# Performance work log

Measured on AMD Instinct MI355X. Metric: run time of the kernel, lower is better.

Reference implementation:

```python
import jax, jax.numpy as jnp
import numpy as np

C = 128; HEADS = 8; GH = 32; GW = 32; B = 8; PD = 8  # PD = (dim//4)//4

def _conv(x, w, pad, dil=1, groups=1):
    return jax.lax.conv_general_dilated(
        x, w, (1, 1), [(pad[0], pad[0]), (pad[1], pad[1])],
        rhs_dilation=(dil, dil),
        dimension_numbers=('NCHW', 'OIHW', 'NCHW'),
        feature_group_count=groups)

def _lrelu(t):
    return jnp.where(t >= 0, t, 0.1 * t)

def _ln(t, g, b, eps=1e-5):
    m = jnp.mean(t, -1, keepdims=True)
    v = jnp.var(t, -1, keepdims=True)
    return (t - m) * jax.lax.rsqrt(v + eps) * g + b

def setup_inputs():
    rng = np.random.RandomState(0)
    f = lambda *s: jnp.asarray((rng.randn(*s) * 0.05).astype(np.float32))
    ones = lambda n: jnp.ones((n,), jnp.float32)
    zeros = lambda n: jnp.zeros((n,), jnp.float32)
    # Swin-style relative position index over the (GH, GW) group
    coords = np.stack(np.meshgrid(np.arange(GH), np.arange(GW), indexing='ij')).reshape(2, -1)
    rel = (coords[:, :, None] - coords[:, None, :]).transpose(1, 2, 0)
    rel[..., 0] += GH - 1; rel[..., 1] += GW - 1; rel[..., 0] *= 2 * GW - 1
    rel_idx = jnp.asarray(rel.sum(-1).astype(np.int32))  # [N, N]
    biases = np.stack(np.meshgrid(np.arange(1 - GH, GH), np.arange(1 - GW, GW), indexing='ij'))
    biases = jnp.asarray(biases.reshape(2, -1).T.astype(np.float32))  # [(2GH-1)*(2GW-1), 2]
    return dict(
        x=jnp.asarray(rng.rand(B, C, GH, GW).astype(np.float32)),
        conv1_w=f(C, C, 3, 3), conv2_w=f(C, C, 3, 3), conv3_w=f(C, C, 3, 3),
        convt_w=f(C, 3, 1, 1),
        rba_w=f(C, C, 3, 1), rba_b=zeros(C), rbb_w=f(C, C, 1, 3), rbb_b=zeros(C),
        pp_w=f(PD, 2), pp_b=zeros(PD),
        l1_g=ones(PD), l1_b=zeros(PD), l1_w=f(PD, PD), l1_b2=zeros(PD),
        l2_g=ones(PD), l2_b=zeros(PD), l2_w=f(PD, PD), l2_b2=zeros(PD),
        l3_g=ones(PD), l3_b=zeros(PD), l3_w=f(HEADS, PD), l3_b2=zeros(HEADS),
        qk_w=f(2 * C, C), qk_b=zeros(2 * C),
        v_w=f(C, C), v_b=zeros(C),
        proj_w=f(C, C), proj_b=zeros(C),
        fc1_w=f(C, C), fc1_b=zeros(C), fc2_w=f(C, C), fc2_b=zeros(C),
        biases=biases, rel_idx=rel_idx,
    )

def reference(x, conv1_w, conv2_w, conv3_w, convt_w, rba_w, rba_b, rbb_w, rbb_b,
              pp_w, pp_b, l1_g, l1_b, l1_w, l1_b2, l2_g, l2_b, l2_w, l2_b2,
              l3_g, l3_b, l3_w, l3_b2, qk_w, qk_b, v_w, v_b, proj_w, proj_b,
              fc1_w, fc1_b, fc2_w, fc2_b, biases, rel_idx):
    Bn, Cc, Hh, Ww = x.shape
    N = Hh * Ww
    hd = Cc // HEADS
    # FeaExtract: ResASPP (3 dilated 3x3 convs, grouped 1x1 merge) + residual
    b1 = _lrelu(_conv(x, conv1_w, (1, 1)))
    b2 = _lrelu(_conv(x, conv2_w, (3, 3), dil=3))
    b3 = _lrelu(_conv(x, conv3_w, (5, 5), dil=5))
    a = _conv(jnp.concatenate([b1, b2, b3], 1), convt_w, (0, 0), groups=Cc) + x
    # RB: (3,1) conv -> lrelu -> (1,3) conv + residual
    r = _lrelu(_conv(a, rba_w, (1, 0)) + rba_b[None, :, None, None])
    r = _conv(r, rbb_w, (0, 1)) + rbb_b[None, :, None, None]
    o0 = r + a
    # original uses in-place clamp_, so o0 is clamped before flattening
    o0 = jnp.clip(o0, 0.0, 1.0)
    E = o0.reshape(Bn, Cc, N).transpose(0, 2, 1)  # [B, N, C]
    qk = E @ qk_w.T + qk_b  # [B, N, 2C]
    q = qk[..., :Cc].reshape(Bn, N, HEADS, hd).transpose(0, 2, 1, 3)
    k = qk[..., Cc:].reshape(Bn, N, HEADS, hd).transpose(0, 2, 1, 3)
    v = (E @ v_w.T + v_b).reshape(Bn, N, HEADS, hd).transpose(0, 2, 1, 3)
    attn = jnp.einsum('bhid,bhjd->bhij', q * (hd ** -0.5), k)
    # DynamicPosBias MLP (residual=False): Linear(2,pd) -> [LN,ReLU,Linear] x2 -> LN,ReLU,Linear(pd,heads)
    p = biases @ pp_w.T + pp_b
    p = jax.nn.relu(_ln(p, l1_g, l1_b)) @ l1_w.T + l1_b2
    p = jax.nn.relu(_ln(p, l2_g, l2_b)) @ l2_w.T + l2_b2
    p = jax.nn.relu(_ln(p, l3_g, l3_b)) @ l3_w.T + l3_b2  # [L, heads]
    rpb = p[rel_idx]  # gather -> [N, N, heads]
    attn = attn + rpb.transpose(2, 0, 1)[None]
    attn = jax.nn.softmax(attn, axis=-1)
    y = jnp.einsum('bhij,bhjd->bhid', attn, v).transpose(0, 2, 1, 3).reshape(Bn, N, Cc) + E
    x_proj = y @ proj_w.T + proj_b
    h = jax.nn.gelu(x_proj @ fc1_w.T + fc1_b, approximate=False)
    return (h @ fc2_w.T + fc2_b) + y
```

## Files before the change

### kernel.cpp

```cpp
#include <hip/hip_runtime.h>
#include <hip/hip_bf16.h>

typedef __hip_bfloat16 bf16;
typedef __bf16 bf16x8 __attribute__((ext_vector_type(8)));
typedef float f32x4 __attribute__((ext_vector_type(4)));

#define Lb 3969

#define XP_F   0
#define WF_F   903168
#define WR_F   1124352
#define WG_F   1173504
#define BH_F   1222656
#define R1P_F  1222656
#define QKV_F  1222656
#define AP_F   2795520
#define YT_F   2795520
#define EB_F   3352576
#define XPT_F  3352576
#define H1T_F  0
#define RPB_F  3876864
#define FLAG_F 3908616
#define RT_F   3908624
#define VT_F   4416528

__device__ __forceinline__ float b2f(bf16 v) { return __bfloat162float(v); }
__device__ __forceinline__ bf16 f2b(float v) { return __float2bfloat16(v); }

template <typename T> __device__ __forceinline__ float ldw(const void* p, int i);
template <> __device__ __forceinline__ float ldw<bf16>(const void* p, int i) {
  return __bfloat162float(((const bf16*)p)[i]);
}
template <> __device__ __forceinline__ float ldw<float>(const void* p, int i) {
  return ((const float*)p)[i];
}
template <typename T> __device__ __forceinline__ void stw(void* p, size_t i, float v);
template <> __device__ __forceinline__ void stw<bf16>(void* p, size_t i, float v) {
  ((bf16*)p)[i] = __float2bfloat16(v);
}
template <> __device__ __forceinline__ void stw<float>(void* p, size_t i, float v) {
  ((float*)p)[i] = v;
}

__device__ __forceinline__ unsigned pkb(float a, float b) {
  bf16 x = __float2bfloat16(a), y = __float2bfloat16(b);
  unsigned short ux = *(unsigned short*)&x, uy = *(unsigned short*)&y;
  return (unsigned)ux | ((unsigned)uy << 16);
}
__device__ __forceinline__ float bf2f_lo(unsigned w) {
  unsigned u = w << 16; return *(float*)&u;
}
__device__ __forceinline__ float bf2f_hi(unsigned w) {
  unsigned u = w & 0xffff0000u; return *(float*)&u;
}

__global__ void detect_kernel(const unsigned int* __restrict__ x,
                              int* __restrict__ flag) {
  if (threadIdx.x == 0) {
    int cnt = 0;
    for (int i = 0; i < 256; ++i) {
      unsigned lo = x[i] & 0xFFFFu;
      if (lo >= 0x3C00u && lo < 0x3F80u) cnt++;
    }
    *flag = (cnt >= 128) ? 1 : 0;
  }
}

template <typename T>
__device__ void wprep_body(const void* w1, const void* w2, const void* w3,
                           bf16* __restrict__ Wf)
{
  int tid = blockIdx.x * 256 + threadIdx.x;
  if (tid >= 3 * 9 * 4 * 8 * 64) return;
  int lane = tid & 63;
  int mt = (tid >> 6) & 7;
  int Kc = (tid >> 9) & 3;
  int rem = tid >> 11;
  int t = rem % 9;
  int br = rem / 9;
  const void* w = (br == 0 ? w1 : (br == 1 ? w2 : w3));
  int o = mt * 16 + (lane & 15);
  int ci0 = Kc * 32 + (lane >> 4) * 8;
#pragma unroll
  for (int j = 0; j < 8; ++j)
    Wf[tid * 8 + j] = f2b(ldw<T>(w, (o * 128 + ci0 + j) * 9 + t));
}

__global__ __launch_bounds__(256) void wprep_kernel(
    const void* w1, const void* w2, const void* w3, bf16* Wf, const int* flag)
{
  if (*flag) wprep_body<bf16>(w1, w2, w3, Wf);
  else       wprep_body<float>(w1, w2, w3, Wf);
}

template <typename T>
__device__ void wprep2_body(const void* rba_w, const void* rbb_w,
                            const void* qk_w, const void* v_w,
                            const void* proj_w, const void* fc1_w,
                            const void* fc2_w, bf16* __restrict__ Wr,
                            bf16* __restrict__ Wg)
{
  int tid = blockIdx.x * 256 + threadIdx.x;
  if (tid >= 24576) return;
  int lane = tid & 63, li = lane & 15, quad = lane >> 4;
  if (tid < 12288) {
    int f = tid;
    int Kc = (f >> 6) & 3, mt = (f >> 8) & 7, q = f >> 11;
    const void* w = (q >= 3) ? rbb_w : rba_w;
    int t = q % 3;
#pragma unroll
    for (int j = 0; j < 8; ++j)
      Wr[(size_t)f * 8 + j] =
          f2b(ldw<T>(w, ((mt * 16 + li) * 128 + Kc * 32 + quad * 8 + j) * 3 + t));
  } else {
    int g = tid - 12288;
    int Kc = (g >> 6) & 3, mtg = g >> 8;
    const void* w; int mrow; float sc = 1.f;
    if (mtg < 16)      { w = qk_w;   mrow = mtg * 16; if (mtg < 8) sc = 0.25f; }
    else if (mtg < 24) { w = v_w;    mrow = (mtg - 16) * 16; }
    else if (mtg < 32) { w = proj_w; mrow = (mtg - 24) * 16; }
    else if (mtg < 40) { w = fc1_w;  mrow = (mtg - 32) * 16; }
    else               { w = fc2_w;  mrow = (mtg - 40) * 16; }
#pragma unroll
    for (int j = 0; j < 8; ++j)
      Wg[(size_t)g * 8 + j] =
          f2b(sc * ldw<T>(w, (mrow + li) * 128 + Kc * 32 + quad * 8 + j));
  }
}

__global__ __launch_bounds__(256) void wprep2_kernel(
    const void* rba_w, const void* rbb_w, const void* qk_w, const void* v_w,
    const void* proj_w, const void* fc1_w, const void* fc2_w,
    bf16* Wr, bf16* Wg, const int* flag)
{
  if (*flag) wprep2_body<bf16>(rba_w, rbb_w, qk_w, v_w, proj_w, fc1_w, fc2_w, Wr, Wg);
  else       wprep2_body<float>(rba_w, rbb_w, qk_w, v_w, proj_w, fc1_w, fc2_w, Wr, Wg);
}

template <typename T>
__device__ void nhwc_body(const void* x, bf16* __restrict__ xp, bf16 (*tile)[128])
{
  const int b = blockIdx.x >> 5;
  const int row = blockIdx.x & 31;
  const int t = threadIdx.x;
  {
    int ci = t >> 1, half = t & 1;
#pragma unroll
    for (int j = 0; j < 16; ++j) {
      int px = half * 16 + j;
      tile[px][ci] = f2b(ldw<T>(x, ((size_t)b * 128 + ci) * 1024 + row * 32 + px));
    }
  }
  __syncthreads();
  {
    int px = t >> 3, c0 = (t & 7) * 16;
    bf16* dst = xp + (((size_t)b * 42 + row + 5) * 42 + (px + 5)) * 128 + c0;
#pragma unroll
    for (int j = 0; j < 16; ++j) dst[j] = tile[px][c0 + j];
  }
}

__global__ __launch_bounds__(256) void nhwc_kernel(const void* x, bf16* xp,
                                                   const int* flag)
{
  __shared__ bf16 tile[32][128];
  if (*flag) nhwc_body<bf16>(x, xp, tile);
  else       nhwc_body<float>(x, xp, tile);
}

__global__ __launch_bounds__(256) void aspp2_kernel(
    const bf16* __restrict__ xp, const bf16* __restrict__ Wf,
    bf16* __restrict__ bh)
{
  const int nt_ = blockIdx.x, br = blockIdx.y >> 1, mh = blockIdx.y & 1;
  const int bb = blockIdx.z;
  const int w = threadIdx.x >> 6, lane = threadIdx.x & 63;
  const int quad = lane >> 4, li = lane & 15;
  const int d = (br == 0 ? 1 : (br == 1 ? 3 : 5));
  const int pxw = nt_ * 64 + w * 16;
  const int y = pxw >> 5, xb = pxw & 31;

  f32x4 acc[4] = {};
  const bf16* Wbase = Wf + (size_t)br * 18432 * 8 + (size_t)mh * 4 * 64 * 8;

  for (int t = 0; t < 9; ++t) {
    const int dy = (t / 3 - 1) * d, dx = (t % 3 - 1) * d;
    const bf16* Asite =
        xp + (((size_t)bb * 42 + (y + 5 + dy)) * 42 + (xb + li + 5 + dx)) * 128;
    const bf16* Wt = Wbase + (size_t)t * 2048 * 8;
#pragma unroll
    for (int Kc = 0; Kc < 4; ++Kc) {
      bf16x8 afrag = *(const bf16x8*)(Asite + Kc * 32 + quad * 8);
      const bf16* Wk = Wt + (size_t)Kc * 512 * 8 + (size_t)lane * 8;
#pragma unroll
      for (int mt = 0; mt < 4; ++mt) {
        bf16x8 wfrag = *(const bf16x8*)(Wk + (size_t)mt * 64 * 8);
        acc[mt] = __builtin_amdgcn_mfma_f32_16x16x32_bf16(afrag, wfrag, acc[mt],
                                                          0, 0, 0);
      }
    }
  }
#pragma unroll
  for (int mt = 0; mt < 4; ++mt)
#pragma unroll
    for (int r = 0; r < 4; ++r) {
      int px = pxw + quad * 4 + r;
      bh[((size_t)bb * 1024 + px) * 384 + br * 128 + (mh * 4 + mt) * 16 + li] =
          f2b(acc[mt][r]);
    }
}

template <typename T>
__device__ void merge2_body(const bf16* __restrict__ xp, const void* wt,
                            const bf16* __restrict__ bh, bf16* __restrict__ ap,
                            float* cw)
{
  const int b = blockIdx.y, px0 = blockIdx.x * 32;
  for (int i = threadIdx.x; i < 384; i += 256) cw[i] = ldw<T>(wt, i);
  __syncthreads();
  const int pxl = threadIdx.x >> 3, og = threadIdx.x & 7;
  const int px = px0 + pxl, o0 = og * 16;
  const int y = px >> 5, x = px & 31;
  const bf16* brow = bh + ((size_t)b * 1024 + px) * 384 + o0 * 3;
  const bf16* xrow = xp + (((size_t)b * 42 + y + 5) * 42 + x + 5) * 128 + o0;
  bf16* arow = ap + (((size_t)b * 34 + y + 1) * 32 + x) * 128 + o0;

  bf16 bl[48], xl[16], ol[16];
#pragma unroll
  for (int k = 0; k < 6; ++k) *(bf16x8*)&bl[k * 8] = *(const bf16x8*)&brow[k * 8];
  *(bf16x8*)&xl[0] = *(const bf16x8*)&xrow[0];
  *(bf16x8*)&xl[8] = *(const bf16x8*)&xrow[8];
#pragma unroll
  for (int j = 0; j < 16; ++j) {
    float v = b2f(xl[j]);
#pragma unroll
    for (int i = 0; i < 3; ++i) {
      float t = b2f(bl[j * 3 + i]);
      v += cw[(o0 + j) * 3 + i] * (t >= 0.f ? t : 0.1f * t);
    }
    ol[j] = f2b(v);
  }
  *(bf16x8*)&arow[0] = *(bf16x8*)&ol[0];
  *(bf16x8*)&arow[8] = *(bf16x8*)&ol[8];
}

__global__ __launch_bounds__(256) void merge2_kernel(
    const bf16* xp, const void* wt, const bf16* bh, bf16* ap, const int* flag)
{
  __shared__ float cw[384];
  if (*flag) merge2_body<bf16>(xp, wt, bh, ap, cw);
  else       merge2_body<float>(xp, wt, bh, ap, cw);
}

template <typename T>
__device__ void rb1_body(const bf16* __restrict__ ap, const bf16* __restrict__ Wr,
                         const void* bias, bf16* __restrict__ r1p)
{
  const int b = blockIdx.z, mh = blockIdx.y;
  const int lane = threadIdx.x;
  const int quad = lane >> 4, li = lane & 15;
  const int pxw = blockIdx.x * 16;
  const int y = pxw >> 5, xb = pxw & 31;
  f32x4 acc[4] = {};
#pragma unroll
  for (int t = 0; t < 3; ++t) {
    const bf16* Asite = ap + (((size_t)b * 34 + y + t) * 32 + xb + li) * 128;
#pragma unroll
    for (int Kc = 0; Kc < 4; ++Kc) {
      bf16x8 afrag = *(const bf16x8*)(Asite + Kc * 32 + quad * 8);
#pragma unroll
      for (int mt = 0; mt < 4; ++mt) {
        int f = (t * 8 + mh * 4 + mt) * 4 + Kc;
        bf16x8 wfrag = *(const bf16x8*)(Wr + ((size_t)f * 64 + lane) * 8);
        acc[mt] = __builtin_amdgcn_mfma_f32_16x16x32_bf16(afrag, wfrag, acc[mt],
                                                          0, 0, 0);
      }
    }
  }
#pragma unroll
  for (int mt = 0; mt < 4; ++mt) {
    int o = (mh * 4 + mt) * 16 + li;
    float bv = ldw<T>(bias, o);
#pragma unroll
    for (int r = 0; r < 4; ++r) {
      int x = xb + quad * 4 + r;
      float v = acc[mt][r] + bv;
      v = (v >= 0.f ? v : 0.1f * v);
      r1p[(((size_t)b * 32 + y) * 34 + x + 1) * 128 + o] = f2b(v);
    }
  }
}

__global__ __launch_bounds__(64) void rb1_kernel(
    const bf16* ap, const bf16* Wr, const void* bias, bf16* r1p, const int* flag)
{
  if (*flag) rb1_body<bf16>(ap, Wr, bias, r1p);
  else       rb1_body<float>(ap, Wr, bias, r1p);
}

template <typename T>
__device__ void rb2_body(const bf16* __restrict__ r1p, const bf16* __restrict__ Wr,
                         const void* bias, const bf16* __restrict__ ap,
                         bf16* __restrict__ Eb)
{
  const int b = blockIdx.z, mh = blockIdx.y;
  const int lane = threadIdx.x;
  const int quad = lane >> 4, li = lane & 15;
  const int pxw = blockIdx.x * 16;
  const int y = pxw >> 5, xb = pxw & 31;
  f32x4 acc[4] = {};
#pragma unroll
  for (int t = 0; t < 3; ++t) {
    const bf16* Asite = r1p + (((size_t)b * 32 + y) * 34 + xb + li + t) * 128;
#pragma unroll
    for (int Kc = 0; Kc < 4; ++Kc) {
      bf16x8 afrag = *(const bf16x8*)(Asite + Kc * 32 + quad * 8);
#pragma unroll
      for (int mt = 0; mt < 4; ++mt) {
        int f = ((3 + t) * 8 + mh * 4 + mt) * 4 + Kc;
        bf16x8 wfrag = *(const bf16x8*)(Wr + ((size_t)f * 64 + lane) * 8);
        acc[mt] = __builtin_amdgcn_mfma_f32_16x16x32_bf16(afrag, wfrag, acc[mt],
                                                          0, 0, 0);
      }
    }
  }
#pragma unroll
  for (int mt = 0; mt < 4; ++mt) {
    int o = (mh * 4 + mt) * 16 + li;
    float bv = ldw<T>(bias, o);
#pragma unroll
    for (int r = 0; r < 4; ++r) {
      int x = xb + quad * 4 + r;
      float v = acc[mt][r] + bv +
                b2f(ap[(((size_t)b * 34 + y + 1) * 32 + x) * 128 + o]);
      v = fminf(fmaxf(v, 0.f), 1.f);
      Eb[((size_t)b * 1024 + y * 32 + x) * 128 + o] = f2b(v);
    }
  }
}

__global__ __launch_bounds__(64) void rb2_kernel(
    const bf16* r1p, const bf16* Wr, const void* bias, const bf16* ap,
    bf16* Eb, const int* flag)
{
  if (*flag) rb2_body<bf16>(r1p, Wr, bias, ap, Eb);
  else       rb2_body<float>(r1p, Wr, bias, ap, Eb);
}

template <typename T>
__device__ __forceinline__ void ln_relu8(const float* t, float* u,
                                         const void* g, const void* bb)
{
  float m = 0.f;
#pragma unroll
  for (int k = 0; k < 8; ++k) m += t[k];
  m *= 0.125f;
  float v = 0.f;
#pragma unroll
  for (int k = 0; k < 8; ++k) { float d = t[k] - m; v += d * d; }
  v *= 0.125f;
  float r = rsqrtf(v + 1e-5f);
#pragma unroll
  for (int k = 0; k < 8; ++k) {
    float val = (t[k] - m) * r * ldw<T>(g, k) + ldw<T>(bb, k);
    u[k] = val > 0.f ? val : 0.f;
  }
}

template <typename T>
__device__ void dpb_body(const void* biases, const void* pp_w, const void* pp_b,
                         const void* l1_g, const void* l1_b, const void* l1_w,
                         const void* l1_b2, const void* l2_g, const void* l2_b,
                         const void* l2_w, const void* l2_b2, const void* l3_g,
                         const void* l3_b, const void* l3_w, const void* l3_b2,
                         float* __restrict__ RPB)
{
  int r = blockIdx.x * 256 + threadIdx.x;
  if (r >= Lb) return;
  float b0 = ldw<T>(biases, r * 2), b1 = ldw<T>(biases, r * 2 + 1);
  float t[8], u[8];
#pragma unroll
  for (int j = 0; j < 8; ++j)
    t[j] = b0 * ldw<T>(pp_w, j * 2) + b1 * ldw<T>(pp_w, j * 2 + 1) +
           ldw<T>(pp_b, j);
  ln_relu8<T>(t, u, l1_g, l1_b);
#pragma unroll
  for (int j = 0; j < 8; ++j) {
    float s = ldw<T>(l1_b2, j);
#pragma unroll
    for (int k = 0; k < 8; ++k) s += u[k] * ldw<T>(l1_w, j * 8 + k);
    t[j] = s;
  }
  ln_relu8<T>(t, u, l2_g, l2_b);
#pragma unroll
  for (int j = 0; j < 8; ++j) {
    float s = ldw<T>(l2_b2, j);
#pragma unroll
    for (int k = 0; k < 8; ++k) s += u[k] * ldw<T>(l2_w, j * 8 + k);
    t[j] = s;
  }
  ln_relu8<T>(t, u, l3_g, l3_b);
#pragma unroll
  for (int h = 0; h < 8; ++h) {
    float s = ldw<T>(l3_b2, h);
#pragma unroll
    for (int k = 0; k < 8; ++k) s += u[k] * ldw<T>(l3_w, h * 8 + k);
    RPB[h * Lb + r] = s;
  }
}

__global__ __launch_bounds__(256) void dpb_kernel(
    const void* biases, const void* pp_w, const void* pp_b, const void* l1_g,
    const void* l1_b, const void* l1_w, const void* l1_b2, const void* l2_g,
    const void* l2_b, const void* l2_w, const void* l2_b2, const void* l3_g,
    const void* l3_b, const void* l3_w, const void* l3_b2, float* RPB,
    const int* flag)
{
  if (*flag)
    dpb_body<bf16>(biases, pp_w, pp_b, l1_g, l1_b, l1_w, l1_b2, l2_g, l2_b,
                   l2_w, l2_b2, l3_g, l3_b, l3_w, l3_b2, RPB);
  else
    dpb_body<float>(biases, pp_w, pp_b, l1_g, l1_b, l1_w, l1_b2, l2_g, l2_b,
                    l2_w, l2_b2, l3_g, l3_b, l3_w, l3_b2, RPB);
}

__global__ __launch_bounds__(64) void rt_kernel(
    const float* __restrict__ RPB, bf16* __restrict__ RT)
{
  const int tt = blockIdx.x, h = blockIdx.y;
  const int t = tt >> 1, p = tt & 1;
  const int lane = threadIdx.x, quad = lane >> 4, li = lane & 15;
  const float* rp = RPB + h * Lb;
#pragma unroll
  for (int mt = 0; mt < 4; ++mt) {
    unsigned w[2];
#pragma unroll
    for (int rr = 0; rr < 2; ++rr) {
      float v0, v1;
#pragma unroll
      for (int k = 0; k < 2; ++k) {
        int r = rr * 2 + k;
        int j = mt * 16 + quad * 4 + r;
        int dy = (t - 30) - (j >> 5);
        int dx = (p * 16 + li) - (j & 31);
        float v = rp[(dy + 31) * 63 + dx + 31];
        if (k == 0) v0 = v; else v1 = v;
      }
      w[rr] = pkb(v0, v1);
    }
    *(uint2*)&RT[(((size_t)h * 124 + tt) * 4 + mt) * 256 + lane * 4] =
        make_uint2(w[0], w[1]);
  }
}

__global__ __launch_bounds__(64) void vt_kernel(
    const bf16* __restrict__ QKV, bf16* __restrict__ VT)
{
  const int c = blockIdx.x, hh = blockIdx.y, b = blockIdx.z;
  __shared__ bf16 Vl[64][20];
  const int lane = threadIdx.x, quad = lane >> 4, li = lane & 15;
  const bf16* vsrc =
      QKV + ((size_t)b * 1024 + c * 64 + lane) * 384 + 256 + hh * 16;
  union { bf16x8 v; uint2 u[2]; } w0, w1;
  w0.v = *(const bf16x8*)vsrc;
  w1.v = *(const bf16x8*)(vsrc + 8);
  *(uint2*)&Vl[lane][0] = w0.u[0];
  *(uint2*)&Vl[lane][4] = w0.u[1];
  *(uint2*)&Vl[lane][8] = w1.u[0];
  *(uint2*)&Vl[lane][12] = w1.u[1];
  __syncthreads();
#pragma unroll
  for (int half = 0; half < 2; ++half) {
    union { bf16 e[8]; bf16x8 v; } uv;
#pragma unroll
    for (int jj = 0; jj < 8; ++jj)
      uv.e[jj] = Vl[half * 32 + quad * 8 + jj][li];
    *(bf16x8*)&VT[((((size_t)(b * 8 + hh) * 16 + c) * 2 + half) * 64 + lane) * 8] =
        uv.v;
  }
}

template <typename T>
__device__ void qkv_body(const bf16* __restrict__ Eb, const bf16* __restrict__ Wg,
                         const void* qk_b, const void* v_b,
                         bf16* __restrict__ QKV)
{
  const int grp = blockIdx.y, b = blockIdx.z;
  const int w = threadIdx.x >> 6, lane = threadIdx.x & 63;
  const int quad = lane >> 4, li = lane & 15;
  const int pxw = blockIdx.x * 64 + w * 16;
  bf16x8 ef[4];
#pragma unroll
  for (int Kc = 0; Kc < 4; ++Kc)
    ef[Kc] = *(const bf16x8*)&Eb[((size_t)b * 1024 + pxw + li) * 128 + Kc * 32 +
                                 quad * 8];
  f32x4 acc[8] = {};
#pragma unroll
  for (int nt = 0; nt < 8; ++nt) {
    int g = grp * 8 + nt;
#pragma unroll
    for (int Kc = 0; Kc < 4; ++Kc) {
      bf16x8 wf = *(const bf16x8*)&Wg[(((size_t)g * 4 + Kc) * 64 + lane) * 8];
      acc[nt] = __builtin_amdgcn_mfma_f32_16x16x32_bf16(ef[Kc], wf, acc[nt],
                                                        0, 0, 0);
    }
  }
#pragma unroll
  for (int nt = 0; nt < 8; ++nt) {
    int g = grp * 8 + nt;
    int o = g * 16 + li;
    float bv;
    if (g < 8)       bv = 0.25f * ldw<T>(qk_b, o);
    else if (g < 16) bv = ldw<T>(qk_b, o);
    else             bv = ldw<T>(v_b, o - 256);
#pragma unroll
    for (int r = 0; r < 4; ++r) {
      int px = pxw + quad * 4 + r;
      QKV[((size_t)b * 1024 + px) * 384 + o] = f2b(acc[nt][r] + bv);
    }
  }
}

__global__ __launch_bounds__(256) void qkv_kernel(
    const bf16* Eb, const bf16* Wg, const void* qk_b, const void* v_b,
    bf16* QKV, const int* flag)
{
  if (*flag) qkv_body<bf16>(Eb, Wg, qk_b, v_b, QKV);
  else       qkv_body<float>(Eb, Wg, qk_b, v_b, QKV);
}

template <typename T, int MODE>
__device__ void mlp_body(const bf16* __restrict__ src, const bf16* __restrict__ Wg,
                         int tb, const void* bias, const bf16* __restrict__ res,
                         void* out)
{
  const int b = blockIdx.z, mh = blockIdx.y;
  const int lane = threadIdx.x;
  const int quad = lane >> 4, li = lane & 15;
  const int pxw = blockIdx.x * 16;
  bf16x8 ef[4];
#pragma unroll
  for (int Kc = 0; Kc < 4; ++Kc)
    ef[Kc] = *(const bf16x8*)&src[((size_t)b * 1024 + pxw + li) * 128 + Kc * 32 +
                                  quad * 8];
  f32x4 acc[2] = {};
#pragma unroll
  for (int nt = 0; nt < 2; ++nt)
#pragma unroll
    for (int Kc = 0; Kc < 4; ++Kc) {
      bf16x8 wf = *(const bf16x8*)&Wg[
          (((size_t)(tb + mh * 2 + nt) * 4 + Kc) * 64 + lane) * 8];
      acc[nt] = __builtin_amdgcn_mfma_f32_16x16x32_bf16(ef[Kc], wf, acc[nt],
                                                        0, 0, 0);
    }
#pragma unroll
  for (int nt = 0; nt < 2; ++nt) {
    int o = (mh * 2 + nt) * 16 + li;
    float bv = ldw<T>(bias, o);
#pragma unroll
    for (int r = 0; r < 4; ++r) {
      int px = pxw + quad * 4 + r;
      float v = acc[nt][r] + bv;
      size_t oidx = ((size_t)b * 1024 + px) * 128 + o;
      if (MODE == 1) v = 0.5f * v * (1.f + erff(v * 0.70710678118f));
      if (MODE == 2) {
        v += b2f(res[oidx]);
        stw<T>(out, oidx, v);
      } else {
        ((bf16*)out)[oidx] = f2b(v);
      }
    }
  }
}

template <int MODE>
__global__ __launch_bounds__(64) void mlp_kernel(
    const bf16* src, const bf16* Wg, int tb, const void* bias, const bf16* res,
    void* out, const int* flag)
{
  if (*flag) mlp_body<bf16, MODE>(src, Wg, tb, bias, res, out);
  else       mlp_body<float, MODE>(src, Wg, tb, bias, res, out);
}

__global__ __launch_bounds__(64) void attn_kernel(
    const bf16* __restrict__ QKV, const bf16* __restrict__ Eb,
    const bf16* __restrict__ RT, const bf16* __restrict__ VT,
    bf16* __restrict__ Yt)
{
  const int qt = blockIdx.x;
  const int hh = blockIdx.y;
  const int b = blockIdx.z;

  __shared__ bf16 Pl[16][72];

  const int lane = threadIdx.x;
  const int quad = lane >> 4, li = lane & 15;
  const int qb = qt * 16;

  const bf16* QKVb = QKV + (size_t)b * 1024 * 384;
  const bf16* VTb = VT + (size_t)(b * 8 + hh) * 16 * 1024;
  const bf16* RTh = RT + (size_t)hh * 124 * 1024;

  bf16x8 qf = (bf16x8){};
  if (quad < 2)
    qf = *(const bf16x8*)&QKVb[(size_t)(qb + li) * 384 + hh * 16 + quad * 8];

  f32x4 O_ = {};
  float m_st = -1e30f, l_st = 0.f;
  const int sbase = (lane & 48) + ((lane >> 2) & 12);

  for (int c = 0; c < 16; ++c) {
    const int c0 = c * 64;
    const int tt = ((qt >> 1) - 2 * c + 30) * 2 + (qt & 1);
    const bf16* rtp = RTh + (size_t)tt * 1024 + lane * 4;

    f32x4 sT[4];
#pragma unroll
    for (int mt = 0; mt < 4; ++mt) {
      uint2 rw = *(const uint2*)(rtp + (size_t)mt * 256);
      f32x4 cin;
      cin[0] = bf2f_lo(rw.x); cin[1] = bf2f_hi(rw.x);
      cin[2] = bf2f_lo(rw.y); cin[3] = bf2f_hi(rw.y);
      bf16x8 kf = (bf16x8){};
      if (quad < 2)
        kf = *(const bf16x8*)&QKVb[(size_t)(c0 + mt * 16 + li) * 384 + 128 +
                                   hh * 16 + quad * 8];
      sT[mt] = __builtin_amdgcn_mfma_f32_16x16x32_bf16(kf, qf, cin, 0, 0, 0);
    }

    float cm = sT[0][0];
#pragma unroll
    for (int mt = 0; mt < 4; ++mt)
#pragma unroll
      for (int r = 0; r < 4; ++r) cm = fmaxf(cm, sT[mt][r]);
    cm = fmaxf(cm, __shfl_xor(cm, 16));
    cm = fmaxf(cm, __shfl_xor(cm, 32));
    float mn = fmaxf(m_st, cm);
    float al = __expf(m_st - mn);
    m_st = mn;
    float ps = 0.f;
#pragma unroll
    for (int mt = 0; mt < 4; ++mt)
#pragma unroll
      for (int r = 0; r < 4; ++r) {
        float p = __expf(sT[mt][r] - mn);
        sT[mt][r] = p;
        ps += p;
      }
    ps += __shfl_xor(ps, 16);
    ps += __shfl_xor(ps, 32);
    l_st = l_st * al + ps;

#pragma unroll
    for (int r = 0; r < 4; ++r) O_[r] *= __shfl(al, sbase + r);

#pragma unroll
    for (int mt = 0; mt < 4; ++mt) {
      uint2 w;
      w.x = pkb(sT[mt][0], sT[mt][1]);
      w.y = pkb(sT[mt][2], sT[mt][3]);
      *(uint2*)&Pl[li][mt * 16 + quad * 4] = w;
    }
    __syncthreads();

#pragma unroll
    for (int half = 0; half < 2; ++half) {
      bf16x8 vf = *(const bf16x8*)&VTb[((size_t)(c * 2 + half) * 64 + lane) * 8];
      bf16x8 pf = *(const bf16x8*)&Pl[li][half * 32 + quad * 8];
      O_ = __builtin_amdgcn_mfma_f32_16x16x32_bf16(pf, vf, O_, 0, 0, 0);
    }
    __syncthreads();
  }

  const bf16* Ebp = Eb + (size_t)b * 1024 * 128 + hh * 16 + li;
  bf16* Ytp = Yt + (size_t)b * 1024 * 128 + hh * 16 + li;
#pragma unroll
  for (int r = 0; r < 4; ++r) {
    float lb = __shfl(l_st, sbase + r);
    int qrow = qb + quad * 4 + r;
    Ytp[(size_t)qrow * 128] =
        f2b(O_[r] / lb + b2f(Ebp[(size_t)qrow * 128]));
  }
}

extern "C" void kernel_launch(void* const* d_in, const int* in_sizes, int n_in,
                              void* d_out, int out_size, void* d_ws,
                              size_t ws_size, hipStream_t stream)
{
  (void)in_sizes; (void)n_in; (void)out_size; (void)ws_size;
  const void* x       = d_in[0];
  const void* conv1_w = d_in[1];
  const void* conv2_w = d_in[2];
  const void* conv3_w = d_in[3];
  const void* convt_w = d_in[4];
  const void* rba_w   = d_in[5];
  const void* rba_b   = d_in[6];
  const void* rbb_w   = d_in[7];
  const void* rbb_b   = d_in[8];
  const void* pp_w    = d_in[9];
  const void* pp_b    = d_in[10];
  const void* l1_g    = d_in[11];
  const void* l1_b    = d_in[12];
  const void* l1_w    = d_in[13];
  const void* l1_b2   = d_in[14];
  const void* l2_g    = d_in[15];
  const void* l2_b    = d_in[16];
  const void* l2_w    = d_in[17];
  const void* l2_b2   = d_in[18];
  const void* l3_g    = d_in[19];
  const void* l3_b    = d_in[20];
  const void* l3_w    = d_in[21];
  const void* l3_b2   = d_in[22];
  const void* qk_w    = d_in[23];
  const void* qk_b    = d_in[24];
  const void* v_w     = d_in[25];
  const void* v_b     = d_in[26];
  const void* proj_w  = d_in[27];
  const void* proj_b  = d_in[28];
  const void* fc1_w   = d_in[29];
  const void* fc1_b   = d_in[30];
  const void* fc2_w   = d_in[31];
  const void* fc2_b   = d_in[32];
  const void* biases  = d_in[33];

  float* ws   = (float*)d_ws;
  bf16*  xp   = (bf16*)(ws + XP_F);
  bf16*  Wf   = (bf16*)(ws + WF_F);
  bf16*  Wr   = (bf16*)(ws + WR_F);
  bf16*  Wg   = (bf16*)(ws + WG_F);
  bf16*  bh   = (bf16*)(ws + BH_F);
  bf16*  r1p  = (bf16*)(ws + R1P_F);
  bf16*  QKV  = (bf16*)(ws + QKV_F);
  bf16*  ap   = (bf16*)(ws + AP_F);
  bf16*  Yt   = (bf16*)(ws + YT_F);
  bf16*  Eb   = (bf16*)(ws + EB_F);
  bf16*  XPt  = (bf16*)(ws + XPT_F);
  bf16*  H1t  = (bf16*)(ws + H1T_F);
  float* RPB  = ws + RPB_F;
  int*   flag = (int*)(ws + FLAG_F);
  bf16*  RT   = (bf16*)(ws + RT_F);
  bf16*  VT   = (bf16*)(ws + VT_F);

  detect_kernel<<<1, 64, 0, stream>>>((const unsigned int*)x, flag);
  wprep_kernel<<<216, 256, 0, stream>>>(conv1_w, conv2_w, conv3_w, Wf, flag);
  wprep2_kernel<<<96, 256, 0, stream>>>(rba_w, rbb_w, qk_w, v_w, proj_w,
                                        fc1_w, fc2_w, Wr, Wg, flag);
  hipMemsetAsync(xp, 0, (size_t)8 * 42 * 42 * 128 * 2, stream);
  nhwc_kernel<<<256, 256, 0, stream>>>(x, xp, flag);
  aspp2_kernel<<<dim3(16, 6, 8), 256, 0, stream>>>(xp, Wf, bh);
  hipMemsetAsync(ap, 0, (size_t)8 * 34 * 32 * 128 * 2, stream);
  merge2_kernel<<<dim3(32, 8), 256, 0, stream>>>(xp, convt_w, bh, ap, flag);
  hipMemsetAsync(r1p, 0, (size_t)8 * 32 * 34 * 128 * 2, stream);
  rb1_kernel<<<dim3(64, 2, 8), 64, 0, stream>>>(ap, Wr, rba_b, r1p, flag);
  rb2_kernel<<<dim3(64, 2, 8), 64, 0, stream>>>(r1p, Wr, rbb_b, ap, Eb, flag);
  dpb_kernel<<<16, 256, 0, stream>>>(biases, pp_w, pp_b, l1_g, l1_b, l1_w,
                                     l1_b2, l2_g, l2_b, l2_w, l2_b2, l3_g,
                                     l3_b, l3_w, l3_b2, RPB, flag);
  rt_kernel<<<dim3(124, 8), 64, 0, stream>>>(RPB, RT);
  qkv_kernel<<<dim3(16, 3, 8), 256, 0, stream>>>(Eb, Wg, qk_b, v_b, QKV, flag);
  vt_kernel<<<dim3(16, 8, 8), 64, 0, stream>>>(QKV, VT);
  attn_kernel<<<dim3(64, 8, 8), 64, 0, stream>>>(QKV, Eb, RT, VT, Yt);
  mlp_kernel<0><<<dim3(64, 4, 8), 64, 0, stream>>>(Yt, Wg, 24, proj_b, nullptr,
                                                   XPt, flag);
  mlp_kernel<1><<<dim3(64, 4, 8), 64, 0, stream>>>(XPt, Wg, 32, fc1_b, nullptr,
                                                   H1t, flag);
  mlp_kernel<2><<<dim3(64, 4, 8), 64, 0, stream>>>(H1t, Wg, 40, fc2_b, Yt,
                                                   d_out, flag);
}
```

Baseline: 256.7 us.

## Merge dtype detect and weight prep kernels, replace memsets with in-kernel halo zeroing

Folds the dtype detection and both weight-prep kernels into one launch, where each wave detects the input dtype locally with a lane reduction. It also removes three full-buffer memsets by having nhwc, merge2 and rb1 zero only the padding halo regions they own. This cuts four to five dispatches and the memset bandwidth. The risk is a missed halo region, since the buffers alias other workspace regions, and every wave now repeats the detect read.

```diff
diff --git a/kernel.cpp b/kernel.cpp
--- a/kernel.cpp
+++ b/kernel.cpp
@@ -54,87 +54,80 @@
   unsigned u = w & 0xffff0000u; return *(float*)&u;
 }
 
-__global__ void detect_kernel(const unsigned int* __restrict__ x,
-                              int* __restrict__ flag) {
-  if (threadIdx.x == 0) {
-    int cnt = 0;
-    for (int i = 0; i < 256; ++i) {
-      unsigned lo = x[i] & 0xFFFFu;
-      if (lo >= 0x3C00u && lo < 0x3F80u) cnt++;
-    }
-    *flag = (cnt >= 128) ? 1 : 0;
-  }
+__device__ __forceinline__ bool detect_local(const unsigned* x) {
+  int lane = threadIdx.x & 63;
+  int cnt = 0;
+#pragma unroll
+  for (int k = 0; k < 4; ++k) {
+    unsigned lo = x[lane + 64 * k] & 0xFFFFu;
+    cnt += (lo >= 0x3C00u && lo < 0x3F80u) ? 1 : 0;
+  }
+#pragma unroll
+  for (int off = 1; off < 64; off <<= 1) cnt += __shfl_xor(cnt, off);
+  return cnt >= 128;
 }
 
 template <typename T>
-__device__ void wprep_body(const void* w1, const void* w2, const void* w3,
-                           bf16* __restrict__ Wf)
+__device__ void wprep_all_body(const void* w1, const void* w2, const void* w3,
+                               const void* rba_w, const void* rbb_w,
+                               const void* qk_w, const void* v_w,
+                               const void* proj_w, const void* fc1_w,
+                               const void* fc2_w, bf16* __restrict__ Wf,
+                               bf16* __restrict__ Wr, bf16* __restrict__ Wg)
 {
   int tid = blockIdx.x * 256 + threadIdx.x;
-  if (tid >= 3 * 9 * 4 * 8 * 64) return;
-  int lane = tid & 63;
-  int mt = (tid >> 6) & 7;
-  int Kc = (tid >> 9) & 3;
-  int rem = tid >> 11;
-  int t = rem % 9;
-  int br = rem / 9;
-  const void* w = (br == 0 ? w1 : (br == 1 ? w2 : w3));
-  int o = mt * 16 + (lane & 15);
-  int ci0 = Kc * 32 + (lane >> 4) * 8;
-#pragma unroll
-  for (int j = 0; j < 8; ++j)
-    Wf[tid * 8 + j] = f2b(ldw<T>(w, (o * 128 + ci0 + j) * 9 + t));
-}
-
-__global__ __launch_bounds__(256) void wprep_kernel(
-    const void* w1, const void* w2, const void* w3, bf16* Wf, const int* flag)
-{
-  if (*flag) wprep_body<bf16>(w1, w2, w3, Wf);
-  else       wprep_body<float>(w1, w2, w3, Wf);
-}
-
-template <typename T>
-__device__ void wprep2_body(const void* rba_w, const void* rbb_w,
-                            const void* qk_w, const void* v_w,
-                            const void* proj_w, const void* fc1_w,
-                            const void* fc2_w, bf16* __restrict__ Wr,
-                            bf16* __restrict__ Wg)
-{
-  int tid = blockIdx.x * 256 + threadIdx.x;
-  if (tid >= 24576) return;
   int lane = tid & 63, li = lane & 15, quad = lane >> 4;
-  if (tid < 12288) {
-    int f = tid;
-    int Kc = (f >> 6) & 3, mt = (f >> 8) & 7, q = f >> 11;
-    const void* w = (q >= 3) ? rbb_w : rba_w;
-    int t = q % 3;
+  if (tid < 55296) {
+    int mt = (tid >> 6) & 7;
+    int Kc = (tid >> 9) & 3;
+    int rem = tid >> 11;
+    int t = rem % 9;
+    int br = rem / 9;
+    const void* w = (br == 0 ? w1 : (br == 1 ? w2 : w3));
+    int o = mt * 16 + li;
+    int ci0 = Kc * 32 + quad * 8;
 #pragma unroll
     for (int j = 0; j < 8; ++j)
-      Wr[(size_t)f * 8 + j] =
-          f2b(ldw<T>(w, ((mt * 16 + li) * 128 + Kc * 32 + quad * 8 + j) * 3 + t));
+      Wf[(size_t)tid * 8 + j] = f2b(ldw<T>(w, (o * 128 + ci0 + j) * 9 + t));
   } else {
-    int g = tid - 12288;
-    int Kc = (g >> 6) & 3, mtg = g >> 8;
-    const void* w; int mrow; float sc = 1.f;
-    if (mtg < 16)      { w = qk_w;   mrow = mtg * 16; if (mtg < 8) sc = 0.25f; }
-    else if (mtg < 24) { w = v_w;    mrow = (mtg - 16) * 16; }
-    else if (mtg < 32) { w = proj_w; mrow = (mtg - 24) * 16; }
-    else if (mtg < 40) { w = fc1_w;  mrow = (mtg - 32) * 16; }
-    else               { w = fc2_w;  mrow = (mtg - 40) * 16; }
-#pragma unroll
-    for (int j = 0; j < 8; ++j)
-      Wg[(size_t)g * 8 + j] =
-          f2b(sc * ldw<T>(w, (mrow + li) * 128 + Kc * 32 + quad * 8 + j));
-  }
-}
-
-__global__ __launch_bounds__(256) void wprep2_kernel(
+    int u = tid - 55296;
+    if (u < 12288) {
+      int Kc = (u >> 6) & 3, mt = (u >> 8) & 7, q = u >> 11;
+      const void* w = (q >= 3) ? rbb_w : rba_w;
+      int t = q % 3;
+#pragma unroll
+      for (int j = 0; j < 8; ++j)
+        Wr[(size_t)u * 8 + j] =
+            f2b(ldw<T>(w, ((mt * 16 + li) * 128 + Kc * 32 + quad * 8 + j) * 3 + t));
+    } else if (u < 24576) {
+      int g = u - 12288;
+      int Kc = (g >> 6) & 3, mtg = g >> 8;
+      const void* w; int mrow; float sc = 1.f;
+      if (mtg < 16)      { w = qk_w;   mrow = mtg * 16; if (mtg < 8) sc = 0.25f; }
+      else if (mtg < 24) { w = v_w;    mrow = (mtg - 16) * 16; }
+      else if (mtg < 32) { w = proj_w; mrow = (mtg - 24) * 16; }
+      else if (mtg < 40) { w = fc1_w;  mrow = (mtg - 32) * 16; }
+      else               { w = fc2_w;  mrow = (mtg - 40) * 16; }
+#pragma unroll
+      for (int j = 0; j < 8; ++j)
+        Wg[(size_t)g * 8 + j] =
+            f2b(sc * ldw<T>(w, (mrow + li) * 128 + Kc * 32 + quad * 8 + j));
+    }
+  }
+}
+
+__global__ __launch_bounds__(256) void wprep_all_kernel(
+    const unsigned* x, const void* w1, const void* w2, const void* w3,
     const void* rba_w, const void* rbb_w, const void* qk_w, const void* v_w,
     const void* proj_w, const void* fc1_w, const void* fc2_w,
-    bf16* Wr, bf16* Wg, const int* flag)
-{
-  if (*flag) wprep2_body<bf16>(rba_w, rbb_w, qk_w, v_w, proj_w, fc1_w, fc2_w, Wr, Wg);
-  else       wprep2_body<float>(rba_w, rbb_w, qk_w, v_w, proj_w, fc1_w, fc2_w, Wr, Wg);
+    bf16* Wf, bf16* Wr, bf16* Wg, int* flag)
+{
+  bool isbf = detect_local(x);
+  if (blockIdx.x == 0 && threadIdx.x == 0) *flag = isbf ? 1 : 0;
+  if (isbf) wprep_all_body<bf16>(w1, w2, w3, rba_w, rbb_w, qk_w, v_w, proj_w,
+                                 fc1_w, fc2_w, Wf, Wr, Wg);
+  else      wprep_all_body<float>(w1, w2, w3, rba_w, rbb_w, qk_w, v_w, proj_w,
+                                  fc1_w, fc2_w, Wf, Wr, Wg);
 }
 
 template <typename T>
@@ -143,6 +136,22 @@
   const int b = blockIdx.x >> 5;
   const int row = blockIdx.x & 31;
   const int t = threadIdx.x;
+  const size_t bbase = (size_t)b * 42 * 42 * 128;
+  const bf16x8 z = (bf16x8){};
+
+  if (t < 160) {
+    int side = t / 80;
+    int off = (t % 80) * 8;
+    *(bf16x8*)&xp[bbase + ((size_t)(row + 5) * 42 + side * 37) * 128 + off] = z;
+  }
+  {
+    int zr = (row < 5) ? row : ((row >= 27) ? row + 10 : -1);
+    if (zr >= 0) {
+      size_t base = bbase + (size_t)zr * 42 * 128;
+      for (int k = t; k < 672; k += 256) *(bf16x8*)&xp[base + k * 8] = z;
+    }
+  }
+
   {
     int ci = t >> 1, half = t & 1;
 #pragma unroll
@@ -154,7 +163,7 @@
   __syncthreads();
   {
     int px = t >> 3, c0 = (t & 7) * 16;
-    bf16* dst = xp + (((size_t)b * 42 + row + 5) * 42 + (px + 5)) * 128 + c0;
+    bf16* dst = xp + (bbase + ((size_t)(row + 5) * 42 + (px + 5)) * 128 + c0);
 #pragma unroll
     for (int j = 0; j < 16; ++j) dst[j] = tile[px][c0 + j];
   }
@@ -216,6 +225,14 @@
                             float* cw)
 {
   const int b = blockIdx.y, px0 = blockIdx.x * 32;
+  const bf16x8 z = (bf16x8){};
+  if (blockIdx.x == 0) {
+    size_t base = ((size_t)b * 34 + 0) * 32 * 128;
+    for (int k = threadIdx.x; k < 512; k += 256) *(bf16x8*)&ap[base + k * 8] = z;
+  } else if (blockIdx.x == 31) {
+    size_t base = ((size_t)b * 34 + 33) * 32 * 128;
+    for (int k = threadIdx.x; k < 512; k += 256) *(bf16x8*)&ap[base + k * 8] = z;
+  }
   for (int i = threadIdx.x; i < 384; i += 256) cw[i] = ldw<T>(wt, i);
   __syncthreads();
   const int pxl = threadIdx.x >> 3, og = threadIdx.x & 7;
@@ -276,6 +293,13 @@
                                                           0, 0, 0);
       }
     }
+  }
+  if (quad == 0) {
+    int xcol = (xb == 0) ? 0 : 33;
+#pragma unroll
+    for (int mt = 0; mt < 4; ++mt)
+      r1p[(((size_t)b * 32 + y) * 34 + xcol) * 128 + (mh * 4 + mt) * 16 + li] =
+          f2b(0.f);
   }
 #pragma unroll
   for (int mt = 0; mt < 4; ++mt) {
@@ -741,16 +765,12 @@
   bf16*  RT   = (bf16*)(ws + RT_F);
   bf16*  VT   = (bf16*)(ws + VT_F);
 
-  detect_kernel<<<1, 64, 0, stream>>>((const unsigned int*)x, flag);
-  wprep_kernel<<<216, 256, 0, stream>>>(conv1_w, conv2_w, conv3_w, Wf, flag);
-  wprep2_kernel<<<96, 256, 0, stream>>>(rba_w, rbb_w, qk_w, v_w, proj_w,
-                                        fc1_w, fc2_w, Wr, Wg, flag);
-  hipMemsetAsync(xp, 0, (size_t)8 * 42 * 42 * 128 * 2, stream);
+  wprep_all_kernel<<<312, 256, 0, stream>>>(
+      (const unsigned*)x, conv1_w, conv2_w, conv3_w, rba_w, rbb_w, qk_w, v_w,
+      proj_w, fc1_w, fc2_w, Wf, Wr, Wg, flag);
   nhwc_kernel<<<256, 256, 0, stream>>>(x, xp, flag);
   aspp2_kernel<<<dim3(16, 6, 8), 256, 0, stream>>>(xp, Wf, bh);
-  hipMemsetAsync(ap, 0, (size_t)8 * 34 * 32 * 128 * 2, stream);
   merge2_kernel<<<dim3(32, 8), 256, 0, stream>>>(xp, convt_w, bh, ap, flag);
-  hipMemsetAsync(r1p, 0, (size_t)8 * 32 * 34 * 128 * 2, stream);
   rb1_kernel<<<dim3(64, 2, 8), 64, 0, stream>>>(ap, Wr, rba_b, r1p, flag);
   rb2_kernel<<<dim3(64, 2, 8), 64, 0, stream>>>(r1p, Wr, rbb_b, ap, Eb, flag);
   dpb_kernel<<<16, 256, 0, stream>>>(biases, pp_w, pp_b, l1_g, l1_b, l1_w,
```

Result: faster. 242.8 us (-5.4%).
